# Optimization experiments

Measured on AMD Instinct MI355X. Metric: run time of the kernel, lower is better.

Reference implementation:

```python
import jax, jax.numpy as jnp
import numpy as np
from jax import lax

NUM_CLASSES = 80
IOU_THR = 0.5
SCORE_THR = 0.5
MAX_BOXES = 100
NEG = jnp.float32(-1e9)


def setup_inputs() -> dict:
    key = jax.random.key(0)
    ks = jax.random.split(key, 9)
    B = 64
    d = {}
    d['bbox13'] = jax.random.uniform(ks[0], (B, 13, 13, 3, 4), dtype=jnp.float32)
    d['p13'] = jax.random.uniform(ks[1], (B, 13, 13, 3, 1), dtype=jnp.float32)
    d['c13'] = jax.random.uniform(ks[2], (B, 13, 13, 3, NUM_CLASSES), dtype=jnp.float32)
    d['bbox26'] = jax.random.uniform(ks[3], (B, 26, 26, 3, 4), dtype=jnp.float32)
    d['p26'] = jax.random.uniform(ks[4], (B, 26, 26, 3, 1), dtype=jnp.float32)
    d['c26'] = jax.random.uniform(ks[5], (B, 26, 26, 3, NUM_CLASSES), dtype=jnp.float32)
    d['bbox52'] = jax.random.uniform(ks[6], (B, 52, 52, 3, 4), dtype=jnp.float32)
    d['p52'] = jax.random.uniform(ks[7], (B, 52, 52, 3, 1), dtype=jnp.float32)
    d['c52'] = jax.random.uniform(ks[8], (B, 52, 52, 3, NUM_CLASSES), dtype=jnp.float32)
    return d


def _nms_single(boxes, scores):
    # boxes: [N, 4] as [y1, x1, y2, x2] (normalized internally like TF), scores: [N]
    y1 = jnp.minimum(boxes[:, 0], boxes[:, 2])
    y2 = jnp.maximum(boxes[:, 0], boxes[:, 2])
    x1 = jnp.minimum(boxes[:, 1], boxes[:, 3])
    x2 = jnp.maximum(boxes[:, 1], boxes[:, 3])
    area = (y2 - y1) * (x2 - x1)
    s0 = jnp.where(scores > SCORE_THR, scores, NEG)

    def step(s, _):
        i = jnp.argmax(s)
        sc = s[i]
        valid = sc > SCORE_THR
        iy1 = jnp.maximum(y1, y1[i]); iy2 = jnp.minimum(y2, y2[i])
        ix1 = jnp.maximum(x1, x1[i]); ix2 = jnp.minimum(x2, x2[i])
        inter = jnp.maximum(iy2 - iy1, 0.0) * jnp.maximum(ix2 - ix1, 0.0)
        union = area + area[i] - inter
        iou = jnp.where(union > 0, inter / union, 0.0)
        s = jnp.where(iou > IOU_THR, NEG, s).at[i].set(NEG)
        return s, (i, sc, valid)

    _, (idx, sel_s, valid) = lax.scan(step, s0, None, length=MAX_BOXES)
    b = jnp.clip(boxes[idx], 0.0, 1.0)          # TF combined NMS: clip_boxes=True
    b = jnp.where(valid[:, None], b, 0.0)       # pad invalid with zeros
    sel_s = jnp.where(valid, sel_s, 0.0)
    cls = jnp.zeros_like(sel_s)                 # single score class -> class id 0
    return b, sel_s, cls, valid.sum().astype(jnp.int32)


def reference(bbox13, p13, c13, bbox26, p26, c26, bbox52, p52, c52):
    B = bbox13.shape[0]
    nc = c13.shape[-1]
    bbox = jnp.concatenate([bbox13.reshape(B, -1, 4), bbox26.reshape(B, -1, 4), bbox52.reshape(B, -1, 4)], axis=1)
    p = jnp.concatenate([p13.reshape(B, -1), p26.reshape(B, -1), p52.reshape(B, -1)], axis=1)
    c = jnp.concatenate([c13.reshape(B, -1, nc), c26.reshape(B, -1, nc), c52.reshape(B, -1, nc)], axis=1)
    cls_idx = jnp.argmax(c, axis=-1).astype(jnp.float32)  # quirky: class *index* scales objectness
    score = p * cls_idx                                     # [B, N]
    b, s, cl, valid = jax.vmap(_nms_single)(bbox, score)
    pred = jnp.concatenate([b, s[..., None], cl[..., None]], axis=-1)  # [B, MAX_BOXES, 6]
    return pred, valid
```

## Files before the change

### kernel.cpp

```cpp
#include <hip/hip_runtime.h>

#define NUM_CLASSES 80
#define N13 507
#define N26 2028
#define N52 8112
#define NANCH (N13 + N26 + N52)
#define BATCH 64
#define MAXB 100
#define NB 3720
#define BOFF 0xFC00u
#define KPT 11
#define TOPK 1024
#define LCAP 4096
#define LMASK (LCAP-1)
#define APB 64

typedef unsigned long long u64;

__device__ __forceinline__ bool sup_cmp(float inter, float un) {
    return (un > 0.f) && ((double)inter > 0x1.000001p-1 * (double)un);
}

__device__ __forceinline__ u64 readlane64(u64 v, int l) {
    unsigned int lo = (unsigned int)__builtin_amdgcn_readlane((int)(v & 0xFFFFFFFFull), l);
    unsigned int hi = (unsigned int)__builtin_amdgcn_readlane((int)(v >> 32), l);
    return ((u64)hi << 32) | (u64)lo;
}

__global__ __launch_bounds__(256) void score_kernel(
    const float* __restrict__ c13, const float* __restrict__ p13,
    const float* __restrict__ c26, const float* __restrict__ p26,
    const float* __restrict__ c52, const float* __restrict__ p52,
    float* __restrict__ scores)
{
    int a   = blockIdx.x * APB + (threadIdx.x >> 2);
    int sub = threadIdx.x & 3;
    int b   = blockIdx.y;
    if (a >= NANCH) return;
    const float* cbase; const float* pbase;
    if (a < N13)            { cbase = c13 + ((size_t)b*N13 + a) * NUM_CLASSES;           pbase = p13 + (size_t)b*N13 + a; }
    else if (a < N13+N26)   { cbase = c26 + ((size_t)b*N26 + (a-N13)) * NUM_CLASSES;     pbase = p26 + (size_t)b*N26 + (a-N13); }
    else                    { cbase = c52 + ((size_t)b*N52 + (a-N13-N26)) * NUM_CLASSES; pbase = p52 + (size_t)b*N52 + (a-N13-N26); }
    float mx = -1.0f; int mi = 0;
    #pragma unroll
    for (int q = 0; q < 5; ++q) {
        float4 v = *(const float4*)(cbase + q*16 + sub*4);
        int cb = q*16 + sub*4;
        if (v.x > mx) { mx = v.x; mi = cb+0; }
        if (v.y > mx) { mx = v.y; mi = cb+1; }
        if (v.z > mx) { mx = v.z; mi = cb+2; }
        if (v.w > mx) { mx = v.w; mi = cb+3; }
    }
    #pragma unroll
    for (int off = 1; off < 4; off <<= 1) {
        float ov = __shfl_xor(mx, off);
        int   oi = __shfl_xor(mi, off);
        if (ov > mx || (ov == mx && oi < mi)) { mx = ov; mi = oi; }
    }
    if (sub == 0) scores[(size_t)b*NANCH + a] = pbase[0] * (float)mi;
}

__device__ __forceinline__ float4 load_box(const float* __restrict__ b13,
                                           const float* __restrict__ b26,
                                           const float* __restrict__ b52,
                                           int b, int n)
{
    if (n < N13)          return *(const float4*)(b13 + ((size_t)b*N13 + n)*4);
    else if (n < N13+N26) return *(const float4*)(b26 + ((size_t)b*N26 + (n-N13))*4);
    else                  return *(const float4*)(b52 + ((size_t)b*N52 + (n-N13-N26))*4);
}

__global__ __launch_bounds__(1024) void nms_sort_scan(
    const float* __restrict__ scores,
    const float* __restrict__ b13, const float* __restrict__ b26, const float* __restrict__ b52,
    float* __restrict__ out)
{
    const int b    = blockIdx.x;
    const int tid  = threadIdx.x;
    const int lane = tid & 63;
    const int wid  = tid >> 6;

    __shared__ u64 lst[LCAP];
    __shared__ unsigned int cnt[NB];
    __shared__ unsigned int wtot[16];
    __shared__ float4 acc4[MAXB];
    __shared__ u64 kmat[64];
    __shared__ u64 sup_lds[16];
    __shared__ float outrec[MAXB][6];
    __shared__ int accN_s, T_s, L_s;

    const float* sc = scores + (size_t)b * NANCH;

    float sreg[KPT];
    #pragma unroll
    for (int k = 0; k < KPT; ++k) {
        int n = tid + (k << 10);
        sreg[k] = (n < NANCH) ? sc[n] : 0.f;
    }

    for (int i = tid; i < NB; i += 1024) cnt[i] = 0u;
    if (tid == 0) accN_s = 0;
    __syncthreads();

    #pragma unroll
    for (int k = 0; k < KPT; ++k) {
        float s = sreg[k];
        if (s > 0.5f) {
            unsigned int bk = (__float_as_uint(s) >> 14) - BOFF;
            if (bk >= NB) bk = NB - 1;
            atomicAdd(&cnt[bk], 1u);
        }
    }
    __syncthreads();

    unsigned int loc[4]; unsigned int s4 = 0u;
    #pragma unroll
    for (int q = 0; q < 4; ++q) {
        int r = tid*4 + q;
        unsigned int v = (r < NB) ? cnt[NB-1-r] : 0u;
        loc[q] = v; s4 += v;
    }
    unsigned int incl = s4;
    #pragma unroll
    for (int off = 1; off < 64; off <<= 1) {
        unsigned int v = __shfl_up(incl, off);
        if (lane >= off) incl += v;
    }
    if (lane == 63) wtot[wid] = incl;
    __syncthreads();
    unsigned int wexcl = 0u, total = 0u;
    #pragma unroll
    for (int w = 0; w < 16; ++w) { unsigned int t = wtot[w]; if (w < wid) wexcl += t; total += t; }
    unsigned int run = wexcl + (incl - s4);
    if (tid == 0) { T_s = 0; L_s = (int)total; }
    __syncthreads();
    #pragma unroll
    for (int q = 0; q < 4; ++q) {
        int r = tid*4 + q;
        if (r < NB) {
            int bk = NB-1-r;
            unsigned int c = loc[q];
            if (run < TOPK && run + c >= TOPK) { T_s = bk; L_s = (int)(run + c); }
            cnt[bk] = run;
            run += c;
        }
    }
    __syncthreads();
    const int total_i = (int)total;
    int Treg = T_s;
    int regionEnd = L_s;

    #pragma unroll
    for (int k = 0; k < KPT; ++k) {
        float s = sreg[k];
        if (s > 0.5f) {
            unsigned int bits = __float_as_uint(s);
            unsigned int bk = (bits >> 14) - BOFF;
            if (bk >= NB) bk = NB - 1;
            if ((int)bk >= Treg) {
                unsigned int pos = atomicAdd(&cnt[bk], 1u);
                lst[pos & LMASK] = ((u64)bits << 32) | (u64)(0xFFFFFFFFu - (unsigned int)(tid + (k<<10)));
            }
        }
    }
    __syncthreads();

    {
        u64 kk[4]; int tt[4];
        #pragma unroll
        for (int i = 0; i < 4; ++i) {
            int p = tid + (i << 10);
            tt[i] = -1; kk[i] = 0ull;
            if (p < regionEnd) {
                u64 key = lst[p & LMASK];
                unsigned int bk = (unsigned int)(key >> 46) - BOFF;
                if (bk >= NB) bk = NB - 1;
                unsigned int st = (bk+1 < NB) ? cnt[bk+1] : 0u;
                unsigned int e  = cnt[bk];
                unsigned int rank = 0u;
                for (unsigned int q = st; q < e; ++q) rank += (lst[q & LMASK] > key) ? 1u : 0u;
                kk[i] = key; tt[i] = (int)(st + rank);
            }
        }
        __syncthreads();
        #pragma unroll
        for (int i = 0; i < 4; ++i) if (tt[i] >= 0) lst[tt[i] & LMASK] = kk[i];
        __syncthreads();
    }

    int accN = 0;
    u64 key = 0ull; float4 bb = make_float4(0.f,0.f,0.f,0.f); float s = 0.f;
    if (lane < regionEnd) {
        key = lst[lane];
        unsigned int n = 0xFFFFFFFFu - (unsigned int)(key & 0xFFFFFFFFull);
        s = __uint_as_float((unsigned int)(key >> 32));
        bb = load_box(b13, b26, b52, b, (int)n);
    }

    int c = 0;
    while (c < total_i && accN < MAXB) {
        while (c + 64 > regionEnd && regionEnd < total_i) {
            int K2 = regionEnd + TOPK;
            if (tid == 0) { T_s = 0; L_s = total_i; }
            __syncthreads();
            for (int bk = tid; bk < Treg; bk += 1024) {
                unsigned int stv = cnt[bk];
                unsigned int ev  = (bk == 0) ? (unsigned int)total_i : cnt[bk-1];
                if (stv < (unsigned int)K2 && ev >= (unsigned int)K2) { T_s = bk; L_s = (int)ev; }
            }
            __syncthreads();
            int T2 = T_s, L2 = L_s;
            #pragma unroll
            for (int k = 0; k < KPT; ++k) {
                float sv = sreg[k];
                if (sv > 0.5f) {
                    unsigned int bits = __float_as_uint(sv);
                    int bk = (int)((bits >> 14) - BOFF);
                    if (bk >= NB) bk = NB - 1;
                    if (bk >= T2 && bk < Treg) {
                        unsigned int pos = atomicAdd(&cnt[bk], 1u);
                        lst[pos & LMASK] = ((u64)bits << 32) | (u64)(0xFFFFFFFFu - (unsigned int)(tid + (k<<10)));
                    }
                }
            }
            __syncthreads();
            {
                u64 kk[4]; int tt[4];
                #pragma unroll
                for (int i = 0; i < 4; ++i) {
                    int p = regionEnd + tid + (i << 10);
                    tt[i] = -1; kk[i] = 0ull;
                    if (p < L2) {
                        u64 k2 = lst[p & LMASK];
                        unsigned int bk = (unsigned int)(k2 >> 46) - BOFF;
                        if (bk >= NB) bk = NB - 1;
                        unsigned int st = (bk+1 < NB) ? cnt[bk+1] : 0u;
                        unsigned int e  = cnt[bk];
                        unsigned int rank = 0u;
                        for (unsigned int q = st; q < e; ++q) rank += (lst[q & LMASK] > k2) ? 1u : 0u;
                        kk[i] = k2; tt[i] = (int)(st + rank);
                    }
                }
                __syncthreads();
                #pragma unroll
                for (int i = 0; i < 4; ++i) if (tt[i] >= 0) lst[tt[i] & LMASK] = kk[i];
                __syncthreads();
            }
            Treg = T2; regionEnd = L2;
            key = 0ull; bb = make_float4(0.f,0.f,0.f,0.f); s = 0.f;
            if (c + lane < regionEnd) {
                key = lst[(c + lane) & LMASK];
                unsigned int n = 0xFFFFFFFFu - (unsigned int)(key & 0xFFFFFFFFull);
                s = __uint_as_float((unsigned int)(key >> 32));
                bb = load_box(b13, b26, b52, b, (int)n);
            }
        }

        int m = regionEnd - c; if (m > 64) m = 64;
        float oy1 = bb.x, ox1 = bb.y, oy2 = bb.z, ox2 = bb.w, cs = s;
        float y1 = fminf(oy1, oy2), y2 = fmaxf(oy1, oy2);
        float x1 = fminf(ox1, ox2), x2 = fmaxf(ox1, ox2);
        float ar = (y2-y1)*(x2-x1);

        int nc = c + 64;
        if (nc + lane < regionEnd) {
            key = lst[(nc + lane) & LMASK];
            unsigned int n = 0xFFFFFFFFu - (unsigned int)(key & 0xFFFFFFFFull);
            s = __uint_as_float((unsigned int)(key >> 32));
            bb = load_box(b13, b26, b52, b, (int)n);
        } else { s = 0.f; bb = make_float4(0.f,0.f,0.f,0.f); }

        bool supp = (lane >= m);
        #pragma unroll 2
        for (int j = wid; j < accN; j += 16) {
            float4 aj = acc4[j];
            float jar = (aj.z - aj.x) * (aj.w - aj.y);
            float iy1=fmaxf(y1,aj.x), iy2=fminf(y2,aj.z);
            float ix1=fmaxf(x1,aj.y), ix2=fminf(x2,aj.w);
            float inter=fmaxf(iy2-iy1,0.f)*fmaxf(ix2-ix1,0.f);
            float un=(ar+jar)-inter;
            supp |= sup_cmp(inter, un);
        }
        u64 bal = __ballot(supp);
        if (lane == 0) sup_lds[wid] = bal;

        #pragma unroll
        for (int q = 0; q < 4; ++q) {
            int rr = wid + (q << 4);
            float ry1=__shfl(y1,rr), rx1=__shfl(x1,rr), ry2=__shfl(y2,rr), rx2=__shfl(x2,rr);
            float rar=__shfl(ar,rr);
            float iy1=fmaxf(y1,ry1), iy2=fminf(y2,ry2);
            float ix1=fmaxf(x1,rx1), ix2=fminf(x2,rx2);
            float inter=fmaxf(iy2-iy1,0.f)*fmaxf(ix2-ix1,0.f);
            float un=(ar+rar)-inter;
            u64 kb = __ballot(sup_cmp(inter, un));
            if (lane == 0) kmat[rr] = kb;
        }
        __syncthreads();

        if (wid == 0) {
            u64 myrow = kmat[lane];
            u64 B = 0ull;
            #pragma unroll
            for (int w = 0; w < 16; ++w) B |= sup_lds[w];
            u64 valid_m = (m >= 64) ? ~0ull : ((1ull << m) - 1ull);
            u64 rem = (~B) & valid_m;
            u64 accmask = 0ull;
            const int start = accN;
            while (rem && accN < MAXB) {
                int j = __builtin_ctzll(rem);
                u64 rowj = readlane64(myrow, j);
                accmask |= (1ull << j);
                rem &= ~rowj;
                rem &= ~(1ull << j);
                accN++;
            }
            if (accmask & (1ull << lane)) {
                int pos = start + (int)__popcll(accmask & ((1ull << lane) - 1ull));
                acc4[pos] = make_float4(y1, x1, y2, x2);
                outrec[pos][0]=fminf(fmaxf(oy1,0.f),1.f);
                outrec[pos][1]=fminf(fmaxf(ox1,0.f),1.f);
                outrec[pos][2]=fminf(fmaxf(oy2,0.f),1.f);
                outrec[pos][3]=fminf(fmaxf(ox2,0.f),1.f);
                outrec[pos][4]=cs;
                outrec[pos][5]=0.f;
            }
            if (lane == 0) accN_s = accN;
        }
        __syncthreads();
        accN = accN_s;
        c += 64;
    }

    const int accNf = accN_s;
    float* outp = out + (size_t)b * (MAXB*6);
    for (int i = tid; i < MAXB*6; i += 1024) {
        int t = i / 6;
        outp[i] = (t < accNf) ? outrec[t][i % 6] : 0.f;
    }
    if (tid == 0) out[(size_t)BATCH*(MAXB*6) + b] = (float)accNf;
}

extern "C" void kernel_launch(void* const* d_in, const int* in_sizes, int n_in,
                              void* d_out, int out_size, void* d_ws, size_t ws_size,
                              hipStream_t stream)
{
    const float* bbox13 = (const float*)d_in[0];
    const float* p13    = (const float*)d_in[1];
    const float* c13    = (const float*)d_in[2];
    const float* bbox26 = (const float*)d_in[3];
    const float* p26    = (const float*)d_in[4];
    const float* c26    = (const float*)d_in[5];
    const float* bbox52 = (const float*)d_in[6];
    const float* p52    = (const float*)d_in[7];
    const float* c52    = (const float*)d_in[8];
    float* out    = (float*)d_out;
    float* scores = (float*)d_ws;

    dim3 g1((NANCH + APB - 1)/APB, BATCH);
    score_kernel<<<g1, 256, 0, stream>>>(c13, p13, c26, p26, c52, p52, scores);
    nms_sort_scan<<<BATCH, 1024, 0, stream>>>(scores, bbox13, bbox26, bbox52, out);
}
```

Baseline: 57.42 us.

## Process two anchors per thread in scoring; make NMS greedy step redundant across waves

The score kernel now handles two anchors per 4-lane group and issues all ten float4 loads before reducing, to raise memory-level parallelism and halve the grid. In the NMS kernel every wave now redundantly runs the greedy accept loop on double-buffered kmat/sup_lds instead of wave 0 doing it and broadcasting accN through shared memory. This removes one __syncthreads per 64-candidate chunk. The cost is duplicated serial work in every wave and concurrent duplicate writes of identical values to acc4/outrec.

```diff
diff --git a/kernel.cpp b/kernel.cpp
--- a/kernel.cpp
+++ b/kernel.cpp
@@ -13,7 +13,6 @@
 #define TOPK 1024
 #define LCAP 4096
 #define LMASK (LCAP-1)
-#define APB 64
 
 typedef unsigned long long u64;
 
@@ -25,6 +24,15 @@
     unsigned int lo = (unsigned int)__builtin_amdgcn_readlane((int)(v & 0xFFFFFFFFull), l);
     unsigned int hi = (unsigned int)__builtin_amdgcn_readlane((int)(v >> 32), l);
     return ((u64)hi << 32) | (u64)lo;
+}
+
+__device__ __forceinline__ void bases_of(int b, int a, const float*& cb, const float*& pb,
+    const float* c13, const float* p13, const float* c26, const float* p26,
+    const float* c52, const float* p52)
+{
+    if (a < N13)          { cb = c13 + ((size_t)b*N13 + a)*NUM_CLASSES;           pb = p13 + (size_t)b*N13 + a; }
+    else if (a < N13+N26) { cb = c26 + ((size_t)b*N26 + (a-N13))*NUM_CLASSES;     pb = p26 + (size_t)b*N26 + (a-N13); }
+    else                  { cb = c52 + ((size_t)b*N52 + (a-N13-N26))*NUM_CLASSES; pb = p52 + (size_t)b*N52 + (a-N13-N26); }
 }
 
 __global__ __launch_bounds__(256) void score_kernel(
@@ -33,31 +41,59 @@
     const float* __restrict__ c52, const float* __restrict__ p52,
     float* __restrict__ scores)
 {
-    int a   = blockIdx.x * APB + (threadIdx.x >> 2);
-    int sub = threadIdx.x & 3;
-    int b   = blockIdx.y;
-    if (a >= NANCH) return;
-    const float* cbase; const float* pbase;
-    if (a < N13)            { cbase = c13 + ((size_t)b*N13 + a) * NUM_CLASSES;           pbase = p13 + (size_t)b*N13 + a; }
-    else if (a < N13+N26)   { cbase = c26 + ((size_t)b*N26 + (a-N13)) * NUM_CLASSES;     pbase = p26 + (size_t)b*N26 + (a-N13); }
-    else                    { cbase = c52 + ((size_t)b*N52 + (a-N13-N26)) * NUM_CLASSES; pbase = p52 + (size_t)b*N52 + (a-N13-N26); }
-    float mx = -1.0f; int mi = 0;
-    #pragma unroll
-    for (int q = 0; q < 5; ++q) {
-        float4 v = *(const float4*)(cbase + q*16 + sub*4);
-        int cb = q*16 + sub*4;
-        if (v.x > mx) { mx = v.x; mi = cb+0; }
-        if (v.y > mx) { mx = v.y; mi = cb+1; }
-        if (v.z > mx) { mx = v.z; mi = cb+2; }
-        if (v.w > mx) { mx = v.w; mi = cb+3; }
-    }
-    #pragma unroll
-    for (int off = 1; off < 4; off <<= 1) {
-        float ov = __shfl_xor(mx, off);
-        int   oi = __shfl_xor(mi, off);
-        if (ov > mx || (ov == mx && oi < mi)) { mx = ov; mi = oi; }
-    }
-    if (sub == 0) scores[(size_t)b*NANCH + a] = pbase[0] * (float)mi;
+    const int cl  = threadIdx.x >> 2;
+    const int sub = threadIdx.x & 3;
+    const int b   = blockIdx.y;
+    const int a0  = blockIdx.x * 128 + cl * 2;
+    const int a1  = a0 + 1;
+    const bool h0 = a0 < NANCH, h1 = a1 < NANCH;
+
+    const float *cb0 = nullptr, *pb0 = nullptr, *cb1 = nullptr, *pb1 = nullptr;
+    if (h0) bases_of(b, a0, cb0, pb0, c13, p13, c26, p26, c52, p52);
+    if (h1) bases_of(b, a1, cb1, pb1, c13, p13, c26, p26, c52, p52);
+
+    float4 va[5], vb[5];
+    #pragma unroll
+    for (int q = 0; q < 5; ++q) va[q] = h0 ? *(const float4*)(cb0 + q*16 + sub*4) : make_float4(-2.f,-2.f,-2.f,-2.f);
+    #pragma unroll
+    for (int q = 0; q < 5; ++q) vb[q] = h1 ? *(const float4*)(cb1 + q*16 + sub*4) : make_float4(-2.f,-2.f,-2.f,-2.f);
+
+    {
+        float mx = -1.0f; int mi = 0;
+        #pragma unroll
+        for (int q = 0; q < 5; ++q) {
+            int cb = q*16 + sub*4;
+            if (va[q].x > mx) { mx = va[q].x; mi = cb+0; }
+            if (va[q].y > mx) { mx = va[q].y; mi = cb+1; }
+            if (va[q].z > mx) { mx = va[q].z; mi = cb+2; }
+            if (va[q].w > mx) { mx = va[q].w; mi = cb+3; }
+        }
+        #pragma unroll
+        for (int off = 1; off < 4; off <<= 1) {
+            float ov = __shfl_xor(mx, off);
+            int   oi = __shfl_xor(mi, off);
+            if (ov > mx || (ov == mx && oi < mi)) { mx = ov; mi = oi; }
+        }
+        if (sub == 0 && h0) scores[(size_t)b*NANCH + a0] = pb0[0] * (float)mi;
+    }
+    {
+        float mx = -1.0f; int mi = 0;
+        #pragma unroll
+        for (int q = 0; q < 5; ++q) {
+            int cb = q*16 + sub*4;
+            if (vb[q].x > mx) { mx = vb[q].x; mi = cb+0; }
+            if (vb[q].y > mx) { mx = vb[q].y; mi = cb+1; }
+            if (vb[q].z > mx) { mx = vb[q].z; mi = cb+2; }
+            if (vb[q].w > mx) { mx = vb[q].w; mi = cb+3; }
+        }
+        #pragma unroll
+        for (int off = 1; off < 4; off <<= 1) {
+            float ov = __shfl_xor(mx, off);
+            int   oi = __shfl_xor(mi, off);
+            if (ov > mx || (ov == mx && oi < mi)) { mx = ov; mi = oi; }
+        }
+        if (sub == 0 && h1) scores[(size_t)b*NANCH + a1] = pb1[0] * (float)mi;
+    }
 }
 
 __device__ __forceinline__ float4 load_box(const float* __restrict__ b13,
@@ -84,10 +120,10 @@
     __shared__ unsigned int cnt[NB];
     __shared__ unsigned int wtot[16];
     __shared__ float4 acc4[MAXB];
-    __shared__ u64 kmat[64];
-    __shared__ u64 sup_lds[16];
+    __shared__ u64 kmat[2][64];
+    __shared__ u64 sup_lds[2][16];
     __shared__ float outrec[MAXB][6];
-    __shared__ int accN_s, T_s, L_s;
+    __shared__ int T_s, L_s;
 
     const float* sc = scores + (size_t)b * NANCH;
 
@@ -99,7 +135,6 @@
     }
 
     for (int i = tid; i < NB; i += 1024) cnt[i] = 0u;
-    if (tid == 0) accN_s = 0;
     __syncthreads();
 
     #pragma unroll
@@ -257,6 +292,7 @@
         }
 
         int m = regionEnd - c; if (m > 64) m = 64;
+        const int par = (c >> 6) & 1;
         float oy1 = bb.x, ox1 = bb.y, oy2 = bb.z, ox2 = bb.w, cs = s;
         float y1 = fminf(oy1, oy2), y2 = fmaxf(oy1, oy2);
         float x1 = fminf(ox1, ox2), x2 = fmaxf(ox1, ox2);
@@ -282,7 +318,7 @@
             supp |= sup_cmp(inter, un);
         }
         u64 bal = __ballot(supp);
-        if (lane == 0) sup_lds[wid] = bal;
+        if (lane == 0) sup_lds[par][wid] = bal;
 
         #pragma unroll
         for (int q = 0; q < 4; ++q) {
@@ -294,15 +330,15 @@
             float inter=fmaxf(iy2-iy1,0.f)*fmaxf(ix2-ix1,0.f);
             float un=(ar+rar)-inter;
             u64 kb = __ballot(sup_cmp(inter, un));
-            if (lane == 0) kmat[rr] = kb;
+            if (lane == 0) kmat[par][rr] = kb;
         }
         __syncthreads();
 
-        if (wid == 0) {
-            u64 myrow = kmat[lane];
+        {
+            u64 myrow = kmat[par][lane];
             u64 B = 0ull;
             #pragma unroll
-            for (int w = 0; w < 16; ++w) B |= sup_lds[w];
+            for (int w = 0; w < 16; ++w) B |= sup_lds[par][w];
             u64 valid_m = (m >= 64) ? ~0ull : ((1ull << m) - 1ull);
             u64 rem = (~B) & valid_m;
             u64 accmask = 0ull;
@@ -325,20 +361,17 @@
                 outrec[pos][4]=cs;
                 outrec[pos][5]=0.f;
             }
-            if (lane == 0) accN_s = accN;
-        }
-        __syncthreads();
-        accN = accN_s;
+        }
         c += 64;
     }
 
-    const int accNf = accN_s;
+    __syncthreads();
     float* outp = out + (size_t)b * (MAXB*6);
     for (int i = tid; i < MAXB*6; i += 1024) {
         int t = i / 6;
-        outp[i] = (t < accNf) ? outrec[t][i % 6] : 0.f;
-    }
-    if (tid == 0) out[(size_t)BATCH*(MAXB*6) + b] = (float)accNf;
+        outp[i] = (t < accN) ? outrec[t][i % 6] : 0.f;
+    }
+    if (tid == 0) out[(size_t)BATCH*(MAXB*6) + b] = (float)accN;
 }
 
 extern "C" void kernel_launch(void* const* d_in, const int* in_sizes, int n_in,
@@ -357,7 +390,7 @@
     float* out    = (float*)d_out;
     float* scores = (float*)d_ws;
 
-    dim3 g1((NANCH + APB - 1)/APB, BATCH);
+    dim3 g1((NANCH + 127)/128, BATCH);
     score_kernel<<<g1, 256, 0, stream>>>(c13, p13, c26, p26, c52, p52, scores);
     nms_sort_scan<<<BATCH, 1024, 0, stream>>>(scores, bbox13, bbox26, bbox52, out);
 }
```

Result: slower. 66.60 us (+16.0%).
